# Optimization experiments

Hardware: AMD Instinct MI355X
Metric: run time of the kernel (lower is better)

The kernel has to match this reference:

```python
import jax, jax.numpy as jnp
import numpy as np

N_EMBD = 1024
N_HEAD = 16
HEAD_DIM = N_EMBD // N_HEAD
EPS = 1e-5


def setup_inputs() -> dict:
    key = jax.random.key(0)
    ks = jax.random.split(key, 6)
    B, S, D = 2, 2048, N_EMBD
    s = 0.02
    return {
        "x": jax.random.normal(ks[0], (B, S, D), jnp.float32),
        "ln1_g": jnp.ones((D,), jnp.float32),
        "ln1_b": jnp.zeros((D,), jnp.float32),
        "w_attn": jax.random.normal(ks[1], (D, 3 * D), jnp.float32) * s,
        "b_attn": jnp.zeros((3 * D,), jnp.float32),
        "w_attn_proj": jax.random.normal(ks[2], (D, D), jnp.float32) * s,
        "b_attn_proj": jnp.zeros((D,), jnp.float32),
        "ln2_g": jnp.ones((D,), jnp.float32),
        "ln2_b": jnp.zeros((D,), jnp.float32),
        "w_fc": jax.random.normal(ks[3], (D, 4 * D), jnp.float32) * s,
        "b_fc": jnp.zeros((4 * D,), jnp.float32),
        "w_fc_proj": jax.random.normal(ks[4], (4 * D, D), jnp.float32) * s,
        "b_fc_proj": jnp.zeros((D,), jnp.float32),
    }


def _layernorm(x, g, b):
    mu = jnp.mean(x, axis=-1, keepdims=True)
    var = jnp.mean(jnp.square(x - mu), axis=-1, keepdims=True)
    return (x - mu) * jax.lax.rsqrt(var + EPS) * g + b


def _block(x, ln1_g, ln1_b, w_attn, b_attn, w_attn_proj, b_attn_proj,
           ln2_g, ln2_b, w_fc, b_fc, w_fc_proj, b_fc_proj):
    B, S, D = x.shape
    h = _layernorm(x, ln1_g, ln1_b)
    qkv = h @ w_attn + b_attn                       # [B,S,3D]
    q, k, v = jnp.split(qkv, 3, axis=-1)
    # [B,H,S,hd]
    q = q.reshape(B, S, N_HEAD, HEAD_DIM).transpose(0, 2, 1, 3)
    k = k.reshape(B, S, N_HEAD, HEAD_DIM).transpose(0, 2, 1, 3)
    v = v.reshape(B, S, N_HEAD, HEAD_DIM).transpose(0, 2, 1, 3)
    scores = jnp.einsum("bhqd,bhkd->bhqk", q, k) / jnp.sqrt(
        jnp.asarray(HEAD_DIM, x.dtype))
    causal = jnp.tril(jnp.ones((S, S), bool))
    scores = jnp.where(causal, scores, -jnp.inf)
    attn = jax.nn.softmax(scores, axis=-1)
    out = jnp.einsum("bhqk,bhkd->bhqd", attn, v)    # [B,H,S,hd]
    out = out.transpose(0, 2, 1, 3).reshape(B, S, D)
    x = x + (out @ w_attn_proj + b_attn_proj)
    h2 = _layernorm(x, ln2_g, ln2_b)
    m = jax.nn.gelu(h2 @ w_fc + b_fc, approximate=False)
    x = x + (m @ w_fc_proj + b_fc_proj)
    return x


def reference(x, ln1_g, ln1_b, w_attn, b_attn, w_attn_proj, b_attn_proj,
              ln2_g, ln2_b, w_fc, b_fc, w_fc_proj, b_fc_proj):
    return _block(x, ln1_g, ln1_b, w_attn, b_attn, w_attn_proj, b_attn_proj,
                  ln2_g, ln2_b, w_fc, b_fc, w_fc_proj, b_fc_proj)
```

## Files before the change

kernel.cpp:

```cpp
#include <hip/hip_runtime.h>
#include <hip/hip_bf16.h>
#include <math.h>

typedef __bf16 bf16_t;
typedef bf16_t bf16x8 __attribute__((ext_vector_type(8)));
typedef float f32x4 __attribute__((ext_vector_type(4)));
typedef unsigned short u16;
typedef u16 ushort8 __attribute__((ext_vector_type(8)));

static __device__ __forceinline__ u16 f2bf(float f) {
    unsigned u = __builtin_bit_cast(unsigned, f);
    u += 0x7FFFu + ((u >> 16) & 1u);
    return (u16)(u >> 16);
}

__global__ __launch_bounds__(256) void ln_kernel(
    const float* __restrict__ x, const float* __restrict__ g,
    const float* __restrict__ be, u16* __restrict__ out)
{
    const int row = blockIdx.x;
    const int tid = threadIdx.x;
    const float4 v = ((const float4*)(x + (long)row * 1024))[tid];
    float s = v.x + v.y + v.z + v.w;
#pragma unroll
    for (int d = 32; d >= 1; d >>= 1) s += __shfl_xor(s, d);
    __shared__ float r1[4], r2[4];
    if ((tid & 63) == 0) r1[tid >> 6] = s;
    __syncthreads();
    const float mean = (r1[0] + r1[1] + r1[2] + r1[3]) * (1.0f / 1024.0f);
    const float dx = v.x - mean, dy = v.y - mean, dz = v.z - mean, dw = v.w - mean;
    float sq = dx * dx + dy * dy + dz * dz + dw * dw;
#pragma unroll
    for (int d = 32; d >= 1; d >>= 1) sq += __shfl_xor(sq, d);
    if ((tid & 63) == 0) r2[tid >> 6] = sq;
    __syncthreads();
    const float var = (r2[0] + r2[1] + r2[2] + r2[3]) * (1.0f / 1024.0f);
    const float rstd = rsqrtf(var + 1e-5f);
    const float4 gg = ((const float4*)g)[tid];
    const float4 bb = ((const float4*)be)[tid];
    ushort4 o;
    o.x = f2bf(dx * rstd * gg.x + bb.x);
    o.y = f2bf(dy * rstd * gg.y + bb.y);
    o.z = f2bf(dz * rstd * gg.z + bb.z);
    o.w = f2bf(dw * rstd * gg.w + bb.w);
    *(ushort4*)&out[(long)row * 1024 + tid * 4] = o;
}

__global__ __launch_bounds__(256) void tcvt_kernel(
    const float* __restrict__ in, u16* __restrict__ outT, int R, int C)
{
    __shared__ float tile[32][33];
    const int tx = threadIdx.x, ty = threadIdx.y;
    const int c0 = blockIdx.x * 32, r0 = blockIdx.y * 32;
#pragma unroll
    for (int i = 0; i < 4; ++i)
        tile[ty + i * 8][tx] = in[(long)(r0 + ty + i * 8) * C + c0 + tx];
    __syncthreads();
#pragma unroll
    for (int i = 0; i < 4; ++i)
        outT[(long)(c0 + ty + i * 8) * R + r0 + tx] = f2bf(tile[tx][ty + i * 8]);
}

template <int BM, int EPI>
static __device__ __forceinline__ void gemm_body(
    const u16* __restrict__ A, const u16* __restrict__ Bt,
    const float* __restrict__ bias, const float* __restrict__ resid,
    void* __restrict__ C, int M, int N, int K)
{
    constexpr int WN = (BM == 128) ? 2 : 4;
    constexpr int MR = 4;
    constexpr int NR = 128 / WN / 16;
    constexpr int AI = BM / 64;
    constexpr int LPW = AI + 2;
    __shared__ __align__(16) u16 As[2][BM * 32];
    __shared__ __align__(16) u16 Bs[2][128 * 32];
    const int tid = threadIdx.x;
    const int lane = tid & 63;
    const int w = tid >> 6;
    const int wm = w / WN, wn = w % WN;
    const int bm = blockIdx.x, bn = blockIdx.y;
    f32x4 acc[MR][NR] = {};

    const u16* Ablk = A + (long)bm * BM * K;
    const u16* Bblk = Bt + (long)bn * 128 * K;
    const int nt = K >> 5;

    auto stage = [&](int buf, int kb) {
#pragma unroll
        for (int i = 0; i < AI; ++i) {
            const int o = (w * AI + i) * 512 + lane * 8;
            const int row = o >> 5, kk = o & 31;
            __builtin_amdgcn_global_load_lds(
                (const __attribute__((address_space(1))) void*)(Ablk + (long)row * K + kb + kk),
                (__attribute__((address_space(3))) void*)(&As[buf][(w * AI + i) * 512]),
                16, 0, 0);
        }
#pragma unroll
        for (int i = 0; i < 2; ++i) {
            const int o = (w * 2 + i) * 512 + lane * 8;
            const int row = o >> 5, kk = o & 31;
            __builtin_amdgcn_global_load_lds(
                (const __attribute__((address_space(1))) void*)(Bblk + (long)row * K + kb + kk),
                (__attribute__((address_space(3))) void*)(&Bs[buf][(w * 2 + i) * 512]),
                16, 0, 0);
        }
    };

    stage(0, 0);
    for (int t = 0; t < nt; ++t) {
        const int cur = t & 1;
        if (t + 1 < nt) {
            stage(cur ^ 1, (t + 1) << 5);
            asm volatile("s_waitcnt vmcnt(%0)" :: "i"(LPW) : "memory");
        } else {
            asm volatile("s_waitcnt vmcnt(0)" ::: "memory");
        }
        __builtin_amdgcn_s_barrier();
        asm volatile("" ::: "memory");

        bf16x8 af[MR], bfr[NR];
#pragma unroll
        for (int m = 0; m < MR; ++m)
            af[m] = *(const bf16x8*)&As[cur][(wm * MR * 16 + m * 16 + (lane & 15)) * 32 + (lane >> 4) * 8];
#pragma unroll
        for (int n = 0; n < NR; ++n)
            bfr[n] = *(const bf16x8*)&Bs[cur][(wn * NR * 16 + n * 16 + (lane & 15)) * 32 + (lane >> 4) * 8];
#pragma unroll
        for (int m = 0; m < MR; ++m)
#pragma unroll
            for (int n = 0; n < NR; ++n)
                acc[m][n] = __builtin_amdgcn_mfma_f32_16x16x32_bf16(af[m], bfr[n], acc[m][n], 0, 0, 0);

        if (t + 1 < nt) {
            asm volatile("" ::: "memory");
            __builtin_amdgcn_s_barrier();
        }
    }

    const int rowBase = bm * BM + wm * MR * 16;
    const int colBase = bn * 128 + wn * NR * 16;
#pragma unroll
    for (int n = 0; n < NR; ++n) {
        const int col = colBase + n * 16 + (lane & 15);
        const float bv = bias[col];
#pragma unroll
        for (int m = 0; m < MR; ++m) {
#pragma unroll
            for (int r = 0; r < 4; ++r) {
                const int row = rowBase + m * 16 + (lane >> 4) * 4 + r;
                float v = acc[m][n][r] + bv;
                if constexpr (EPI == 1) {
                    const float u = v + 0.044715f * v * v * v;
                    v = v / (1.0f + __expf(-1.5957691216057308f * u));
                }
                if constexpr (EPI == 3) {
                    if (col < 1024) v *= 0.125f;
                }
                if constexpr (EPI == 2) {
                    ((float*)C)[(long)row * N + col] = v + resid[(long)row * N + col];
                } else {
                    ((u16*)C)[(long)row * N + col] = f2bf(v);
                }
            }
        }
    }
}

__global__ __launch_bounds__(256) void gemm_qkv(
    const u16* A, const u16* Bt, const float* bias, const float* resid,
    void* C, int M, int N, int K) { gemm_body<128, 3>(A, Bt, bias, resid, C, M, N, K); }
__global__ __launch_bounds__(256) void gemm_fc(
    const u16* A, const u16* Bt, const float* bias, const float* resid,
    void* C, int M, int N, int K) { gemm_body<128, 1>(A, Bt, bias, resid, C, M, N, K); }
__global__ __launch_bounds__(256) void gemm_ap(
    const u16* A, const u16* Bt, const float* bias, const float* resid,
    void* C, int M, int N, int K) { gemm_body<64, 2>(A, Bt, bias, resid, C, M, N, K); }
__global__ __launch_bounds__(256) void gemm_fp(
    const u16* A, const u16* Bt, const float* bias, const float* resid,
    void* C, int M, int N, int K) { gemm_body<64, 2>(A, Bt, bias, resid, C, M, N, K); }

__global__ __launch_bounds__(256) void attn_kernel(
    const u16* __restrict__ qkv, u16* __restrict__ outb)
{
    const int S = 2048;
    const int ipair = blockIdx.x;
    const int bh = blockIdx.y;
    const int b = bh >> 4, h = bh & 15;
    const int tid = threadIdx.x, lane = tid & 63, w = tid >> 6;
    __shared__ __align__(16) u16 Ks[2][64 * 72];
    __shared__ __align__(16) u16 Vs[2][64 * 72];
    __shared__ __align__(16) u16 Ps[4][16 * 72];

    const long base = (long)b * S * 3072;
    const int rstage = tid >> 3;
    const int cg = (tid & 7) * 8;
    const int sw = cg;
    const u16* kbase = qkv + base + 1024 + h * 64 + cg;
    const u16* vbase = qkv + base + 2048 + h * 64 + cg;

    for (int half = 0; half < 2; ++half) {
        const int qt = half ? 31 - ipair : ipair;
        const int q0 = qt * 64;

        bf16x8 qf[2];
        {
            const int qrow = q0 + w * 16 + (lane & 15);
#pragma unroll
            for (int c = 0; c < 2; ++c)
                qf[c] = *(const bf16x8*)&qkv[base + (long)qrow * 3072 + h * 64 + c * 32 + (lane >> 4) * 8];
        }

        f32x4 Of[4] = {};
        float m = -1e30f, l = 0.0f;

        ushort8 kr[2], vr[2];
#pragma unroll
        for (int it = 0; it < 2; ++it) {
            const long ro = (long)(it * 32 + rstage) * 3072;
            kr[it] = *(const ushort8*)&kbase[ro];
            vr[it] = *(const ushort8*)&vbase[ro];
        }
        __syncthreads();
#pragma unroll
        for (int it = 0; it < 2; ++it) {
            const int r = it * 32 + rstage;
            *(ushort8*)&Ks[0][r * 72 + cg] = kr[it];
#pragma unroll
            for (int j = 0; j < 8; ++j)
                Vs[0][(cg + j) * 72 + (r ^ sw)] = vr[it][j];
        }

        for (int kt = 0; kt <= qt; ++kt) {
            const int cur = kt & 1;
            if (kt < qt) {
#pragma unroll
                for (int it = 0; it < 2; ++it) {
                    const long ro = (long)((kt + 1) * 64 + it * 32 + rstage) * 3072;
                    kr[it] = *(const ushort8*)&kbase[ro];
                    vr[it] = *(const ushort8*)&vbase[ro];
                }
            }
            __syncthreads();

            f32x4 Sf[4] = {};
#pragma unroll
            for (int f = 0; f < 4; ++f) {
#pragma unroll
                for (int c = 0; c < 2; ++c) {
                    const bf16x8 kf = *(const bf16x8*)&Ks[cur][(f * 16 + (lane & 15)) * 72 + c * 32 + (lane >> 4) * 8];
                    Sf[f] = __builtin_amdgcn_mfma_f32_16x16x32_bf16(kf, qf[c], Sf[f], 0, 0, 0);
                }
            }
            if (kt == qt) {
                const int ql = w * 16 + (lane & 15);
#pragma unroll
                for (int f = 0; f < 4; ++f) {
#pragma unroll
                    for (int r = 0; r < 4; ++r) {
                        const int kvl = f * 16 + ((lane >> 4) << 2) + r;
                        if (kvl > ql) Sf[f][r] = -1e30f;
                    }
                }
            }
            float pmax = Sf[0][0];
#pragma unroll
            for (int f = 0; f < 4; ++f)
#pragma unroll
                for (int r = 0; r < 4; ++r) pmax = fmaxf(pmax, Sf[f][r]);
            if (!__all(pmax <= m + 8.0f)) {
                float pm = pmax;
                pm = fmaxf(pm, __shfl_xor(pm, 16));
                pm = fmaxf(pm, __shfl_xor(pm, 32));
                const float mnew = fmaxf(m, pm);
                const float sc = __expf(m - mnew);
                m = mnew;
                l *= sc;
                float sco[4];
#pragma unroll
                for (int r = 0; r < 4; ++r)
                    sco[r] = __shfl(sc, ((lane >> 4) << 2) + r);
#pragma unroll
                for (int f = 0; f < 4; ++f)
#pragma unroll
                    for (int r = 0; r < 4; ++r) Of[f][r] *= sco[r];
            }
            float osum = 0.0f;
#pragma unroll
            for (int f = 0; f < 4; ++f)
#pragma unroll
                for (int r = 0; r < 4; ++r) {
                    const float e = __expf(Sf[f][r] - m);
                    Sf[f][r] = e;
                    osum += e;
                }
            l += osum;
#pragma unroll
            for (int f = 0; f < 4; ++f) {
                const unsigned lo = (unsigned)f2bf(Sf[f][0]) | ((unsigned)f2bf(Sf[f][1]) << 16);
                const unsigned hi = (unsigned)f2bf(Sf[f][2]) | ((unsigned)f2bf(Sf[f][3]) << 16);
                uint2 pk; pk.x = lo; pk.y = hi;
                *(uint2*)&Ps[w][(lane & 15) * 72 + f * 16 + ((lane >> 4) << 2)] = pk;
            }
#pragma unroll
            for (int f = 0; f < 4; ++f) {
                const int hd = f * 16 + (lane & 15);
#pragma unroll
                for (int c = 0; c < 2; ++c) {
                    const int k0 = c * 32 + (lane >> 4) * 8;
                    const bf16x8 pa = *(const bf16x8*)&Ps[w][(lane & 15) * 72 + k0];
                    const bf16x8 vb = *(const bf16x8*)&Vs[cur][hd * 72 + (k0 ^ (hd & 56))];
                    Of[f] = __builtin_amdgcn_mfma_f32_16x16x32_bf16(pa, vb, Of[f], 0, 0, 0);
                }
            }
            if (kt < qt) {
#pragma unroll
                for (int it = 0; it < 2; ++it) {
                    const int r = it * 32 + rstage;
                    *(ushort8*)&Ks[cur ^ 1][r * 72 + cg] = kr[it];
#pragma unroll
                    for (int j = 0; j < 8; ++j)
                        Vs[cur ^ 1][(cg + j) * 72 + (r ^ sw)] = vr[it][j];
                }
            }
        }

        float lt = l;
        lt += __shfl_xor(lt, 16);
        lt += __shfl_xor(lt, 32);
        const float linv = 1.0f / lt;
        float inv[4];
#pragma unroll
        for (int r = 0; r < 4; ++r)
            inv[r] = __shfl(linv, ((lane >> 4) << 2) + r);
#pragma unroll
        for (int f = 0; f < 4; ++f) {
            const int col = h * 64 + f * 16 + (lane & 15);
#pragma unroll
            for (int r = 0; r < 4; ++r) {
                const int qrow = q0 + w * 16 + (lane >> 4) * 4 + r;
                outb[((long)b * S + qrow) * 1024 + col] = f2bf(Of[f][r] * inv[r]);
            }
        }
    }
}

extern "C" void kernel_launch(void* const* d_in, const int* in_sizes, int n_in,
                              void* d_out, int out_size, void* d_ws, size_t ws_size,
                              hipStream_t stream) {
    const float* x      = (const float*)d_in[0];
    const float* ln1_g  = (const float*)d_in[1];
    const float* ln1_b  = (const float*)d_in[2];
    const float* w_attn = (const float*)d_in[3];
    const float* b_attn = (const float*)d_in[4];
    const float* w_ap   = (const float*)d_in[5];
    const float* b_ap   = (const float*)d_in[6];
    const float* ln2_g  = (const float*)d_in[7];
    const float* ln2_b  = (const float*)d_in[8];
    const float* w_fc   = (const float*)d_in[9];
    const float* b_fc   = (const float*)d_in[10];
    const float* w_fp   = (const float*)d_in[11];
    const float* b_fp   = (const float*)d_in[12];
    float* out = (float*)d_out;

    const int R = 4096;
    char* p = (char*)d_ws;
    u16*   wTa  = (u16*)(p);
    u16*   wTap = (u16*)(p + 6291456);
    u16*   wTfc = (u16*)(p + 8388608);
    u16*   wTfp = (u16*)(p + 16777216);
    u16*   hao  = (u16*)(p + 25165824);
    u16*   qkv  = (u16*)(p + 33554432);
    u16*   mb   = hao;
    u16*   h2   = wTa;
    float* x1   = out;

    const dim3 tb(32, 8);
    tcvt_kernel<<<dim3(3072 / 32, 1024 / 32), tb, 0, stream>>>(w_attn, wTa, 1024, 3072);
    tcvt_kernel<<<dim3(1024 / 32, 1024 / 32), tb, 0, stream>>>(w_ap, wTap, 1024, 1024);
    tcvt_kernel<<<dim3(4096 / 32, 1024 / 32), tb, 0, stream>>>(w_fc, wTfc, 1024, 4096);
    tcvt_kernel<<<dim3(1024 / 32, 4096 / 32), tb, 0, stream>>>(w_fp, wTfp, 4096, 1024);

    ln_kernel<<<R, 256, 0, stream>>>(x, ln1_g, ln1_b, hao);
    gemm_qkv<<<dim3(32, 24), 256, 0, stream>>>(hao, wTa, b_attn, nullptr, qkv, R, 3072, 1024);
    attn_kernel<<<dim3(16, 32), 256, 0, stream>>>(qkv, hao);
    gemm_ap<<<dim3(64, 8), 256, 0, stream>>>(hao, wTap, b_ap, x, x1, R, 1024, 1024);
    ln_kernel<<<R, 256, 0, stream>>>(x1, ln2_g, ln2_b, h2);
    gemm_fc<<<dim3(32, 32), 256, 0, stream>>>(h2, wTfc, b_fc, nullptr, mb, R, 4096, 1024);
    gemm_fp<<<dim3(64, 8), 256, 0, stream>>>(mb, wTfp, b_fp, x1, out, R, 1024, 4096);
}
```

Baseline: 271.5 us.

## Deepen GEMM LDS pipeline to multi-stage and remap workgroups across XCDs

GEMM shared-memory staging moves from double buffering to a configurable depth of 3 or 4 stages. The next tile is now issued after the barrier, which removes the trailing barrier per k-step, and vmcnt waits are tuned to the depth. Workgroup indices in both the GEMMs and attention are permuted so consecutive tiles land on the same XCD, improving L2 locality. This costs more LDS per block, which may lower occupancy, and the remap assumes grid sizes divisible by 8.

```diff
diff --git a/kernel.cpp b/kernel.cpp
--- a/kernel.cpp
+++ b/kernel.cpp
@@ -61,7 +61,7 @@
         outT[(long)(c0 + ty + i * 8) * R + r0 + tx] = f2bf(tile[tx][ty + i * 8]);
 }
 
-template <int BM, int EPI>
+template <int BM, int EPI, int DP>
 static __device__ __forceinline__ void gemm_body(
     const u16* __restrict__ A, const u16* __restrict__ Bt,
     const float* __restrict__ bias, const float* __restrict__ resid,
@@ -72,13 +72,16 @@
     constexpr int NR = 128 / WN / 16;
     constexpr int AI = BM / 64;
     constexpr int LPW = AI + 2;
-    __shared__ __align__(16) u16 As[2][BM * 32];
-    __shared__ __align__(16) u16 Bs[2][128 * 32];
+    __shared__ __align__(16) u16 As[DP][BM * 32];
+    __shared__ __align__(16) u16 Bs[DP][128 * 32];
     const int tid = threadIdx.x;
     const int lane = tid & 63;
     const int w = tid >> 6;
     const int wm = w / WN, wn = w % WN;
-    const int bm = blockIdx.x, bn = blockIdx.y;
+    const int nwg = gridDim.x * gridDim.y;
+    const int flat = blockIdx.x + gridDim.x * blockIdx.y;
+    const int work = (flat & 7) * (nwg >> 3) + (flat >> 3);
+    const int bm = work % gridDim.x, bn = work / gridDim.x;
     f32x4 acc[MR][NR] = {};
 
     const u16* Ablk = A + (long)bm * BM * K;
@@ -106,11 +109,14 @@
         }
     };
 
-    stage(0, 0);
+#pragma unroll
+    for (int s = 0; s < DP - 1; ++s) stage(s, s << 5);
+
     for (int t = 0; t < nt; ++t) {
-        const int cur = t & 1;
-        if (t + 1 < nt) {
-            stage(cur ^ 1, (t + 1) << 5);
+        const int cur = t % DP;
+        if (t + DP - 2 < nt) {
+            asm volatile("s_waitcnt vmcnt(%0)" :: "i"((DP - 2) * LPW) : "memory");
+        } else if (t + 1 < nt) {
             asm volatile("s_waitcnt vmcnt(%0)" :: "i"(LPW) : "memory");
         } else {
             asm volatile("s_waitcnt vmcnt(0)" ::: "memory");
@@ -118,6 +124,8 @@
         __builtin_amdgcn_s_barrier();
         asm volatile("" ::: "memory");
 
+        if (t + DP - 1 < nt) stage((t + DP - 1) % DP, (t + DP - 1) << 5);
+
         bf16x8 af[MR], bfr[NR];
 #pragma unroll
         for (int m = 0; m < MR; ++m)
@@ -130,11 +138,7 @@
 #pragma unroll
             for (int n = 0; n < NR; ++n)
                 acc[m][n] = __builtin_amdgcn_mfma_f32_16x16x32_bf16(af[m], bfr[n], acc[m][n], 0, 0, 0);
-
-        if (t + 1 < nt) {
-            asm volatile("" ::: "memory");
-            __builtin_amdgcn_s_barrier();
-        }
+        asm volatile("" ::: "memory");
     }
 
     const int rowBase = bm * BM + wm * MR * 16;
@@ -168,23 +172,25 @@
 
 __global__ __launch_bounds__(256) void gemm_qkv(
     const u16* A, const u16* Bt, const float* bias, const float* resid,
-    void* C, int M, int N, int K) { gemm_body<128, 3>(A, Bt, bias, resid, C, M, N, K); }
+    void* C, int M, int N, int K) { gemm_body<128, 3, 3>(A, Bt, bias, resid, C, M, N, K); }
 __global__ __launch_bounds__(256) void gemm_fc(
     const u16* A, const u16* Bt, const float* bias, const float* resid,
-    void* C, int M, int N, int K) { gemm_body<128, 1>(A, Bt, bias, resid, C, M, N, K); }
+    void* C, int M, int N, int K) { gemm_body<128, 1, 3>(A, Bt, bias, resid, C, M, N, K); }
 __global__ __launch_bounds__(256) void gemm_ap(
     const u16* A, const u16* Bt, const float* bias, const float* resid,
-    void* C, int M, int N, int K) { gemm_body<64, 2>(A, Bt, bias, resid, C, M, N, K); }
+    void* C, int M, int N, int K) { gemm_body<64, 2, 4>(A, Bt, bias, resid, C, M, N, K); }
 __global__ __launch_bounds__(256) void gemm_fp(
     const u16* A, const u16* Bt, const float* bias, const float* resid,
-    void* C, int M, int N, int K) { gemm_body<64, 2>(A, Bt, bias, resid, C, M, N, K); }
+    void* C, int M, int N, int K) { gemm_body<64, 2, 4>(A, Bt, bias, resid, C, M, N, K); }
 
 __global__ __launch_bounds__(256) void attn_kernel(
     const u16* __restrict__ qkv, u16* __restrict__ outb)
 {
     const int S = 2048;
-    const int ipair = blockIdx.x;
-    const int bh = blockIdx.y;
+    const int flat = blockIdx.x + 16 * blockIdx.y;
+    const int work = (flat & 7) * 64 + (flat >> 3);
+    const int ipair = work & 15;
+    const int bh = work >> 4;
     const int b = bh >> 4, h = bh & 15;
     const int tid = threadIdx.x, lane = tid & 63, w = tid >> 6;
     __shared__ __align__(16) u16 Ks[2][64 * 72];
```

New measurement: 271.0 us. Within noise of the previous version (-0.2%).
